# Kernel tuning notes

Hardware: AMD Instinct MI355X
Metric: run time of the kernel (lower is better)

## Reference

```python
import jax, jax.numpy as jnp
import numpy as np

N = 100000      # nodes
E = 1600000     # edges
IN_DIM = 256
H = 128         # hidden_mlp == hidden_gnn
Z = 32          # latent_dim
HD = 128        # hidden_dec


def _lin(k, fan_in, fan_out):
    # torch nn.Linear default init: U(-1/sqrt(fan_in), 1/sqrt(fan_in))
    kw, kb = jax.random.split(k)
    lim = 1.0 / np.sqrt(fan_in)
    W = jax.random.uniform(kw, (fan_in, fan_out), jnp.float32, -lim, lim)
    b = jax.random.uniform(kb, (fan_out,), jnp.float32, -lim, lim)
    return W, b


def setup_inputs() -> dict:
    key = jax.random.key(0)
    ks = jax.random.split(key, 16)
    x = jax.random.normal(ks[0], (N, IN_DIM), jnp.float32)
    edge_index = jax.random.randint(ks[1], (2, E), 0, N, jnp.int64)
    edge_attr = jax.random.uniform(ks[2], (E,), jnp.float32)

    W1, b1 = _lin(ks[3], IN_DIM, H)       # encoder mlp layer 1
    W2, b2 = _lin(ks[4], H, H)            # encoder mlp layer 2
    Wrel1, brel1 = _lin(ks[5], H, H)      # gnn1 lin_rel
    Wroot1, _ = _lin(ks[6], H, H)         # gnn1 lin_root (no bias)
    Wrel2, brel2 = _lin(ks[7], H, H)      # gnn2 lin_rel
    Wroot2, _ = _lin(ks[8], H, H)         # gnn2 lin_root
    Wmu, bmu = _lin(ks[9], H, Z)
    Wlv, blv = _lin(ks[10], H, Z)
    Wd1, bd1 = _lin(ks[11], Z, HD)
    Wd2, bd2 = _lin(ks[12], HD, IN_DIM)
    eps = jax.random.normal(ks[13], (N, Z), jnp.float32)  # reparam noise (fixed)

    return dict(x=x, edge_index=edge_index, edge_attr=edge_attr,
                W1=W1, b1=b1, W2=W2, b2=b2,
                Wrel1=Wrel1, brel1=brel1, Wroot1=Wroot1,
                Wrel2=Wrel2, brel2=brel2, Wroot2=Wroot2,
                Wmu=Wmu, bmu=bmu, Wlv=Wlv, blv=blv,
                Wd1=Wd1, bd1=bd1, Wd2=Wd2, bd2=bd2, eps=eps)


def _graph_conv(h, src, dst, w, Wrel, brel, Wroot):
    # PyG GraphConv (aggr='add'): out_i = lin_rel(sum_{j->i} w_ji * h_j) + lin_root(h_i)
    msgs = h[src] * w[:, None]                       # [E, H] gather
    agg = jax.ops.segment_sum(msgs, dst, num_segments=N)  # [N, H] scatter-add
    return agg @ Wrel + brel + h @ Wroot


def reference(x, edge_index, edge_attr,
              W1, b1, W2, b2,
              Wrel1, brel1, Wroot1,
              Wrel2, brel2, Wroot2,
              Wmu, bmu, Wlv, blv,
              Wd1, bd1, Wd2, bd2, eps):
    src, dst = edge_index[0], edge_index[1]
    # encoder MLP
    h = jax.nn.relu(x @ W1 + b1)
    h = jax.nn.relu(h @ W2 + b2)
    # two GraphConv message-passing layers with ReLU
    h = jax.nn.relu(_graph_conv(h, src, dst, edge_attr, Wrel1, brel1, Wroot1))
    h = jax.nn.relu(_graph_conv(h, src, dst, edge_attr, Wrel2, brel2, Wroot2))
    # heads
    mu = h @ Wmu + bmu
    logvar = h @ Wlv + blv
    # reparameterize with fixed eps
    z = mu + eps * jnp.exp(0.5 * logvar)
    # decoder MLP
    x_recon = jax.nn.relu(z @ Wd1 + bd1) @ Wd2 + bd2
    return x_recon, mu, logvar, z
```

## Files before the change

### kernel.cpp

```cpp
#include <hip/hip_runtime.h>
#include <math.h>

#define NN 100000
#define EE 1600000
#define NB 1563

typedef _Float16 f16;
typedef __attribute__((ext_vector_type(2))) _Float16 f16x2;
typedef __attribute__((ext_vector_type(8))) _Float16 f16x8;
typedef __attribute__((ext_vector_type(4))) float f32x4;
typedef unsigned int u32;

__device__ __forceinline__ float frelu(float v){ return v > 0.f ? v : 0.f; }

__device__ __forceinline__ f32x4 mfma16(f16x8 a, f16x8 b, f32x4 c){
    return __builtin_amdgcn_mfma_f32_16x16x32_f16(a, b, c, 0, 0, 0);
}

__device__ __forceinline__ int2 nt_load_int2(const int2* p){
    long long v = __builtin_nontemporal_load((const long long*)p);
    int2 r; r.x = (int)(v & 0xFFFFFFFFll); r.y = (int)(v >> 32);
    return r;
}

__global__ __launch_bounds__(256) void hist_pack(const int* __restrict__ dst,
                                                 int* __restrict__ blockhist,
                                                 const float* __restrict__ W1,
                                                 const float* __restrict__ W2,
                                                 const float* __restrict__ Wrel1,
                                                 const float* __restrict__ Wroot1,
                                                 const float* __restrict__ Wrel2,
                                                 const float* __restrict__ Wroot2,
                                                 const float* __restrict__ Wd1,
                                                 const float* __restrict__ Wd2,
                                                 const float* __restrict__ Wmu,
                                                 const float* __restrict__ Wlv,
                                                 f16* __restrict__ pack)
{
    __shared__ int cntS[NB];
    const int t = threadIdx.x;
    if (blockIdx.x < 250) {
        const int blk = blockIdx.x;
        for (int i = t; i < NB; i += 256) cntS[i] = 0;
        __syncthreads();
        const int ebase = blk * 6400;
        #pragma unroll
        for (int i = 0; i < 25; i++) {
            int k = dst[ebase + i * 256 + t] >> 6;
            atomicAdd(&cntS[k], 1);
        }
        __syncthreads();
        for (int i = t; i < NB; i += 256)
            blockhist[blk * NB + i] = cntS[i];
        return;
    }
    int tt = (blockIdx.x - 250) * 256 + t;
    float v;
    if (tt < 32768) {
        int l = tt;
        int j = l & 7, lane = (l >> 3) & 63, ct = (l >> 9) & 7, kk = l >> 12;
        int k = kk * 32 + ((lane >> 4) << 3) + j, c = (ct << 4) + (lane & 15);
        v = W1[k * 128 + c];
    } else if (tt < 49152) {
        int l = tt - 32768;
        int j = l & 7, lane = (l >> 3) & 63, ct = (l >> 9) & 7, kk = l >> 12;
        int k = kk * 32 + ((lane >> 4) << 3) + j, c = (ct << 4) + (lane & 15);
        v = W2[k * 128 + c];
    } else if (tt < 81920) {
        int l = tt - 49152;
        int j = l & 7, lane = (l >> 3) & 63, ct = (l >> 9) & 7, kk = l >> 12;
        int k = kk * 32 + ((lane >> 4) << 3) + j, c = (ct << 4) + (lane & 15);
        v = (k < 128) ? Wrel1[k * 128 + c] : Wroot1[(k - 128) * 128 + c];
    } else if (tt < 114688) {
        int l = tt - 81920;
        int j = l & 7, lane = (l >> 3) & 63, ct = (l >> 9) & 7, kk = l >> 12;
        int k = kk * 32 + ((lane >> 4) << 3) + j, c = (ct << 4) + (lane & 15);
        v = (k < 128) ? Wrel2[k * 128 + c] : Wroot2[(k - 128) * 128 + c];
    } else if (tt < 118784) {
        int l = tt - 114688;
        int j = l & 7, lane = (l >> 3) & 63, ct = (l >> 9) & 7;
        int k = ((lane >> 4) << 3) + j, c = (ct << 4) + (lane & 15);
        v = Wd1[k * 128 + c];
    } else if (tt < 151552) {
        int l = tt - 118784;
        int j = l & 7, lane = (l >> 3) & 63, ct = (l >> 9) & 15, kk = l >> 13;
        int k = kk * 32 + ((lane >> 4) << 3) + j, c = (ct << 4) + (lane & 15);
        v = Wd2[k * 256 + c];
    } else {
        int l = tt - 151552;
        int j = l & 7, lane = (l >> 3) & 63, ct = (l >> 9) & 3, kk = l >> 11;
        int k = kk * 32 + ((lane >> 4) << 3) + j, c = (ct << 4) + (lane & 15);
        v = (c < 32) ? Wmu[k * 32 + c] : Wlv[k * 32 + (c - 32)];
    }
    pack[tt] = (f16)v;
}

template<int C>
__device__ __forceinline__ void stage_tile(const float* __restrict__ src, int nbase,
                                           f16* lds, int ldr, int colofs)
{
    const int t = threadIdx.x;
    #pragma unroll
    for (int i = 0; i < (64 * C / 4) / 256; i++) {
        int elem = t + i * 256;
        int row = elem / (C / 4);
        int c4  = elem % (C / 4);
        int srow = nbase + row; if (srow >= NN) srow = NN - 1;
        float4 v = *(const float4*)(src + (size_t)srow * C + c4 * 4);
        union { f16 h[4]; uint2 u; } cv;
        cv.h[0] = (f16)v.x; cv.h[1] = (f16)v.y; cv.h[2] = (f16)v.z; cv.h[3] = (f16)v.w;
        *(uint2*)&lds[row * ldr + colofs + c4 * 4] = cv.u;
    }
}

template<int C>
__device__ __forceinline__ void stage_tile_f16(const f16* __restrict__ src, int nbase,
                                               f16* lds, int ldr, int colofs)
{
    const int t = threadIdx.x;
    #pragma unroll
    for (int i = 0; i < (64 * C / 4) / 256; i++) {
        int elem = t + i * 256;
        int row = elem / (C / 4);
        int c4  = elem % (C / 4);
        int srow = nbase + row; if (srow >= NN) srow = NN - 1;
        uint2 v = *(const uint2*)(src + (size_t)srow * C + c4 * 4);
        *(uint2*)&lds[row * ldr + colofs + c4 * 4] = v;
    }
}

template<int K, int CT>
__device__ __forceinline__ void wave_gemm(const f16* lds, int ldr,
                                          const f16x8* __restrict__ wp, f32x4 acc[CT])
{
    const int lane = threadIdx.x & 63;
    const int wrow = (threadIdx.x >> 6) * 16;
    const int arow = wrow + (lane & 15);
    const int kofs = (lane >> 4) << 3;
    #pragma unroll
    for (int kk = 0; kk < K / 32; kk++) {
        f16x8 a = *(const f16x8*)&lds[arow * ldr + kk * 32 + kofs];
        #pragma unroll
        for (int ct = 0; ct < CT; ct++) {
            f16x8 b = wp[(kk * CT + ct) * 64 + lane];
            acc[ct] = mfma16(a, b, acc[ct]);
        }
    }
}

template<int CT>
__device__ __forceinline__ void zacc(f32x4 acc[CT])
{
    #pragma unroll
    for (int ct = 0; ct < CT; ct++) acc[ct] = f32x4{0.f, 0.f, 0.f, 0.f};
}

template<int CT, bool RELU>
__device__ __forceinline__ void store_f32(float* __restrict__ dst, int OUTC, int nbase,
                                          const float* __restrict__ bias, f32x4 acc[CT])
{
    const int lane = threadIdx.x & 63;
    const int wrow = (threadIdx.x >> 6) * 16;
    #pragma unroll
    for (int ct = 0; ct < CT; ct++) {
        int c = ct * 16 + (lane & 15);
        float bv = bias[c];
        #pragma unroll
        for (int r = 0; r < 4; r++) {
            int node = nbase + wrow + ((lane >> 4) << 2) + r;
            if (node < NN) {
                float v = acc[ct][r] + bv;
                if (RELU) v = frelu(v);
                dst[(size_t)node * OUTC + c] = v;
            }
        }
    }
}

template<int CT, bool RELU>
__device__ __forceinline__ void store_f16g(f16* __restrict__ dst, int OUTC, int nbase,
                                           const float* __restrict__ bias, f32x4 acc[CT])
{
    const int lane = threadIdx.x & 63;
    const int wrow = (threadIdx.x >> 6) * 16;
    #pragma unroll
    for (int ct = 0; ct < CT; ct++) {
        int c = ct * 16 + (lane & 15);
        float bv = bias[c];
        #pragma unroll
        for (int r = 0; r < 4; r++) {
            int node = nbase + wrow + ((lane >> 4) << 2) + r;
            if (node < NN) {
                float v = acc[ct][r] + bv;
                if (RELU) v = frelu(v);
                dst[(size_t)node * OUTC + c] = (f16)v;
            }
        }
    }
}

template<int CT>
__device__ __forceinline__ void store_lds_f16(f16* lds, int ldr,
                                              const float* __restrict__ bias, f32x4 acc[CT])
{
    const int lane = threadIdx.x & 63;
    const int wrow = (threadIdx.x >> 6) * 16;
    #pragma unroll
    for (int ct = 0; ct < CT; ct++) {
        int c = ct * 16 + (lane & 15);
        float bv = bias[c];
        #pragma unroll
        for (int r = 0; r < 4; r++) {
            int row = wrow + ((lane >> 4) << 2) + r;
            lds[row * ldr + c] = (f16)frelu(acc[ct][r] + bv);
        }
    }
}

__global__ __launch_bounds__(256) void colscan_enc(int* __restrict__ blockhist,
                                                   int* __restrict__ totals,
                                                   const float* __restrict__ x,
                                                   const f16x8* __restrict__ wp1,
                                                   const f16x8* __restrict__ wp2,
                                                   const float* __restrict__ b1,
                                                   const float* __restrict__ b2,
                                                   f16* __restrict__ out)
{
    __shared__ __align__(16) f16 shbuf[64 * 264 + 64 * 136];
    const int t = threadIdx.x;
    if (blockIdx.x < NB) {
        int* lds = (int*)shbuf;
        const int k = blockIdx.x;
        int v = (t < 250) ? blockhist[t * NB + k] : 0;
        lds[t] = v;
        __syncthreads();
        for (int off = 1; off < 256; off <<= 1) {
            int y = (t >= off) ? lds[t - off] : 0;
            __syncthreads();
            lds[t] += y;
            __syncthreads();
        }
        if (t < 250) blockhist[t * NB + k] = lds[t] - v;
        if (t == 255) totals[k] = lds[255];
        return;
    }
    f16* xs = shbuf;
    f16* h1 = shbuf + 64 * 264;
    const int nbase = (blockIdx.x - NB) * 64;
    stage_tile<256>(x, nbase, xs, 264, 0);
    __syncthreads();
    f32x4 acc[8];
    zacc<8>(acc);
    wave_gemm<256, 8>(xs, 264, wp1, acc);
    store_lds_f16<8>(h1, 136, b1, acc);
    __syncthreads();
    zacc<8>(acc);
    wave_gemm<128, 8>(h1, 136, wp2, acc);
    store_f16g<8, true>(out, 128, nbase, b2, acc);
}

__global__ __launch_bounds__(256) void scatter(const int* __restrict__ src,
                                               const int* __restrict__ dst,
                                               const float* __restrict__ ea,
                                               const int* __restrict__ totals,
                                               const int* __restrict__ blockhist,
                                               int* __restrict__ bs_g,
                                               int2* __restrict__ tmp)
{
    __shared__ int bsS[NB + 1];
    __shared__ int tmpS[256];
    __shared__ int carryS;
    __shared__ int prefS[NB];
    __shared__ int cntS[NB];
    const int t = threadIdx.x, blk = blockIdx.x;
    if (t == 0) carryS = 0;
    __syncthreads();
    for (int c = 0; c < 7; c++) {
        int idx = c * 256 + t;
        int val = (idx < NB) ? totals[idx] : 0;
        tmpS[t] = val;
        __syncthreads();
        for (int off = 1; off < 256; off <<= 1) {
            int y = (t >= off) ? tmpS[t - off] : 0;
            __syncthreads();
            tmpS[t] += y;
            __syncthreads();
        }
        if (idx < NB) bsS[idx] = carryS + tmpS[t] - val;
        __syncthreads();
        if (t == 255) carryS += tmpS[255];
        __syncthreads();
    }
    if (t == 0) bsS[NB] = carryS;
    for (int i = t; i < NB; i += 256) {
        prefS[i] = blockhist[blk * NB + i];
        cntS[i] = 0;
    }
    __syncthreads();
    if (blk == 0)
        for (int i = t; i < NB + 1; i += 256) bs_g[i] = bsS[i];
    const int ebase = blk * 6400;
    #pragma unroll
    for (int i = 0; i < 25; i++) {
        int e = ebase + i * 256 + t;
        int d = dst[e];
        int k = d >> 6;
        int rank = atomicAdd(&cntS[k], 1);
        int pos = bsS[k] + prefS[k] + rank;
        tmp[pos] = make_int2(src[e] | ((d & 63) << 17), __float_as_int(ea[e]));
    }
}

__global__ __launch_bounds__(256) void bucket_sort(const int2* __restrict__ tmp,
                                                   const int* __restrict__ bs_g,
                                                   int2* __restrict__ pairs,
                                                   int* __restrict__ offsets,
                                                   int* __restrict__ counts)
{
    __shared__ int hist[64], excl[64], cursor[64];
    const int t = threadIdx.x, k = blockIdx.x;
    const int start = bs_g[k], end = bs_g[k + 1];
    if (t < 64) hist[t] = 0;
    __syncthreads();
    for (int i = start + t; i < end; i += 256)
        atomicAdd(&hist[(tmp[i].x >> 17) & 63], 1);
    __syncthreads();
    if (t == 0) {
        int run = 0;
        #pragma unroll
        for (int j = 0; j < 64; j++) { excl[j] = run; cursor[j] = run; run += hist[j]; }
    }
    __syncthreads();
    for (int i = start + t; i < end; i += 256) {
        int2 e = tmp[i];
        int local = (e.x >> 17) & 63;
        int rank = atomicAdd(&cursor[local], 1);
        pairs[start + rank] = make_int2(e.x & 0x1FFFF, e.y);
    }
    if (t < 64) {
        int node = (k << 6) + t;
        if (node < NN) {
            counts[node]  = hist[t];
            offsets[node] = start + excl[t] + hist[t];
        }
    }
}

__global__ __launch_bounds__(256) void agg_q(const f16* __restrict__ h,
                                             const int2* __restrict__ pairs,
                                             const int* __restrict__ offsets,
                                             const int* __restrict__ counts,
                                             f16* __restrict__ out)
{
    const int gt   = blockIdx.x * 256 + threadIdx.x;
    const int node = gt >> 4;
    const int ch   = gt & 15;
    const int end  = offsets[node];
    int i = end - counts[node];
    float acc[8];
    #pragma unroll
    for (int j = 0; j < 8; j++) acc[j] = 0.f;
    const uint4* __restrict__ h16 = (const uint4*)h;
    for (; i + 8 <= end; i += 8) {
        int2 p[8];
        uint4 r[8];
        #pragma unroll
        for (int u = 0; u < 8; u++) p[u] = nt_load_int2(pairs + i + u);
        #pragma unroll
        for (int u = 0; u < 8; u++) r[u] = h16[(size_t)p[u].x * 16 + ch];
        #pragma unroll
        for (int u = 0; u < 8; u++) {
            float w = __int_as_float(p[u].y);
            const f16* e = (const f16*)&r[u];
            #pragma unroll
            for (int j = 0; j < 8; j++) acc[j] = fmaf(w, (float)e[j], acc[j]);
        }
    }
    for (; i + 4 <= end; i += 4) {
        int2 p0 = nt_load_int2(pairs + i);
        int2 p1 = nt_load_int2(pairs + i + 1);
        int2 p2 = nt_load_int2(pairs + i + 2);
        int2 p3 = nt_load_int2(pairs + i + 3);
        uint4 r0 = h16[(size_t)p0.x * 16 + ch];
        uint4 r1 = h16[(size_t)p1.x * 16 + ch];
        uint4 r2 = h16[(size_t)p2.x * 16 + ch];
        uint4 r3 = h16[(size_t)p3.x * 16 + ch];
        float w0 = __int_as_float(p0.y), w1 = __int_as_float(p1.y);
        float w2 = __int_as_float(p2.y), w3 = __int_as_float(p3.y);
        const f16* e0 = (const f16*)&r0;
        const f16* e1 = (const f16*)&r1;
        const f16* e2 = (const f16*)&r2;
        const f16* e3 = (const f16*)&r3;
        #pragma unroll
        for (int j = 0; j < 8; j++) acc[j] = fmaf(w0, (float)e0[j], acc[j]);
        #pragma unroll
        for (int j = 0; j < 8; j++) acc[j] = fmaf(w1, (float)e1[j], acc[j]);
        #pragma unroll
        for (int j = 0; j < 8; j++) acc[j] = fmaf(w2, (float)e2[j], acc[j]);
        #pragma unroll
        for (int j = 0; j < 8; j++) acc[j] = fmaf(w3, (float)e3[j], acc[j]);
    }
    for (; i < end; ++i) {
        int2 p0 = nt_load_int2(pairs + i);
        uint4 r0 = h16[(size_t)p0.x * 16 + ch];
        float w0 = __int_as_float(p0.y);
        const f16* e0 = (const f16*)&r0;
        #pragma unroll
        for (int j = 0; j < 8; j++) acc[j] = fmaf(w0, (float)e0[j], acc[j]);
    }
    union { f16 hh[8]; uint4 u; } cv;
    #pragma unroll
    for (int j = 0; j < 8; j++) cv.hh[j] = (f16)acc[j];
    ((uint4*)out)[(size_t)node * 16 + ch] = cv.u;
}

__global__ __launch_bounds__(256) void conv_mfma(const f16* __restrict__ agg,
                                                 const f16* __restrict__ h,
                                                 const f16x8* __restrict__ wp,
                                                 const float* __restrict__ brel,
                                                 f16* __restrict__ out)
{
    __shared__ __align__(16) f16 as_[64 * 264];
    const int nbase = blockIdx.x * 64;
    stage_tile_f16<128>(agg, nbase, as_, 264, 0);
    stage_tile_f16<128>(h,   nbase, as_, 264, 128);
    __syncthreads();
    f32x4 acc[8];
    zacc<8>(acc);
    wave_gemm<256, 8>(as_, 264, wp, acc);
    store_f16g<8, true>(out, 128, nbase, brel, acc);
}

__global__ __launch_bounds__(256) void tail2_mfma(const f16* __restrict__ h,
                                                  const f16x8* __restrict__ wp_hd,
                                                  const float* __restrict__ bmu,
                                                  const float* __restrict__ blv,
                                                  const f16x8* __restrict__ wp_d1,
                                                  const float* __restrict__ bd1,
                                                  const f16x8* __restrict__ wp_d2,
                                                  const float* __restrict__ bd2,
                                                  const float* __restrict__ eps,
                                                  float* __restrict__ out)
{
    __shared__ __align__(16) f16 hsA[64 * 136];
    __shared__ __align__(16) float muS[64 * 32];
    __shared__ __align__(16) float lvS[64 * 32];
    __shared__ __align__(16) f16 zf[64 * 40];
    const int nbase = blockIdx.x * 64;
    const int t = threadIdx.x;
    const int lane = t & 63;
    const int wrow = (t >> 6) * 16;

    stage_tile_f16<128>(h, nbase, hsA, 136, 0);
    __syncthreads();

    f32x4 acc4[4];
    zacc<4>(acc4);
    wave_gemm<128, 4>(hsA, 136, wp_hd, acc4);
    #pragma unroll
    for (int ct = 0; ct < 4; ct++) {
        int c = ct * 16 + (lane & 15);
        bool ismu = (c < 32);
        int cc = c & 31;
        float bv = ismu ? bmu[cc] : blv[cc];
        float* gbase = out + (ismu ? (size_t)25600000 : (size_t)28800000);
        float* sb = ismu ? muS : lvS;
        #pragma unroll
        for (int r = 0; r < 4; r++) {
            int row = wrow + ((lane >> 4) << 2) + r;
            int node = nbase + row;
            float v = acc4[ct][r] + bv;
            sb[row * 32 + cc] = v;
            if (node < NN) gbase[(size_t)node * 32 + cc] = v;
        }
    }
    __syncthreads();

    {
        const int node = t >> 2;
        const int ch0  = (t & 3) * 8;
        const int gn = nbase + node;
        const float* mu = &muS[node * 32 + ch0];
        const float* lv = &lvS[node * 32 + ch0];
        float4 e0 = make_float4(0.f, 0.f, 0.f, 0.f), e1 = e0;
        if (gn < NN) {
            const size_t g = (size_t)gn * 32 + ch0;
            e0 = *(const float4*)(eps + g);
            e1 = *(const float4*)(eps + g + 4);
        }
        float zv[8];
        zv[0] = fmaf(e0.x, expf(0.5f * lv[0]), mu[0]);
        zv[1] = fmaf(e0.y, expf(0.5f * lv[1]), mu[1]);
        zv[2] = fmaf(e0.z, expf(0.5f * lv[2]), mu[2]);
        zv[3] = fmaf(e0.w, expf(0.5f * lv[3]), mu[3]);
        zv[4] = fmaf(e1.x, expf(0.5f * lv[4]), mu[4]);
        zv[5] = fmaf(e1.y, expf(0.5f * lv[5]), mu[5]);
        zv[6] = fmaf(e1.z, expf(0.5f * lv[6]), mu[6]);
        zv[7] = fmaf(e1.w, expf(0.5f * lv[7]), mu[7]);
        if (gn < NN) {
            const size_t g = (size_t)gn * 32 + ch0;
            *(float4*)(out + 32000000 + g)     = make_float4(zv[0], zv[1], zv[2], zv[3]);
            *(float4*)(out + 32000000 + g + 4) = make_float4(zv[4], zv[5], zv[6], zv[7]);
        }
        #pragma unroll
        for (int j = 0; j < 8; j++) zf[node * 40 + ch0 + j] = (f16)zv[j];
    }
    __syncthreads();

    f32x4 acc8[8];
    zacc<8>(acc8);
    wave_gemm<32, 8>(zf, 40, wp_d1, acc8);
    store_lds_f16<8>(hsA, 136, bd1, acc8);
    __syncthreads();

    f32x4 acc16[16];
    zacc<16>(acc16);
    wave_gemm<128, 16>(hsA, 136, wp_d2, acc16);
    store_f32<16, false>(out, 256, nbase, bd2, acc16);
}

extern "C" void kernel_launch(void* const* d_in, const int* in_sizes, int n_in,
                              void* d_out, int out_size, void* d_ws, size_t ws_size,
                              hipStream_t stream)
{
    const float* x     = (const float*)d_in[0];
    const int*   ei    = (const int*)d_in[1];
    const float* ea    = (const float*)d_in[2];
    const float* W1    = (const float*)d_in[3];
    const float* b1    = (const float*)d_in[4];
    const float* W2    = (const float*)d_in[5];
    const float* b2    = (const float*)d_in[6];
    const float* Wrel1 = (const float*)d_in[7];
    const float* brel1 = (const float*)d_in[8];
    const float* Wroot1= (const float*)d_in[9];
    const float* Wrel2 = (const float*)d_in[10];
    const float* brel2 = (const float*)d_in[11];
    const float* Wroot2= (const float*)d_in[12];
    const float* Wmu   = (const float*)d_in[13];
    const float* bmu   = (const float*)d_in[14];
    const float* Wlv   = (const float*)d_in[15];
    const float* blv   = (const float*)d_in[16];
    const float* Wd1   = (const float*)d_in[17];
    const float* bd1   = (const float*)d_in[18];
    const float* Wd2   = (const float*)d_in[19];
    const float* bd2   = (const float*)d_in[20];
    const float* eps   = (const float*)d_in[21];
    float* out = (float*)d_out;

    char* ws = (char*)d_ws;
    int*  totals    = (int*) (ws);
    int*  blockhist = (int*) (ws + 8192);
    int*  bs_g      = (int*) (ws + 1571200);
    int2* tmp       = (int2*)(ws + 1577472);
    int2* pairs     = (int2*)(ws + 14377472);
    int*  offsets   = (int*) (ws + 27177472);
    int*  counts    = (int*) (ws + 27577472);
    f16*  pack      = (f16*) (ws + 27977472);
    f16*  B0        = (f16*) (ws + 28311552);
    f16*  B1        = (f16*) (ws + 53911552);

    const f16x8* wp_enc1  = (const f16x8*)(pack);
    const f16x8* wp_enc2  = (const f16x8*)(pack + 32768);
    const f16x8* wp_conv1 = (const f16x8*)(pack + 49152);
    const f16x8* wp_conv2 = (const f16x8*)(pack + 81920);
    const f16x8* wp_dec1  = (const f16x8*)(pack + 114688);
    const f16x8* wp_dec2  = (const f16x8*)(pack + 118784);
    const f16x8* wp_heads = (const f16x8*)(pack + 151552);

    const int* src = ei;
    const int* dst = ei + EE;

    hist_pack<<<874, 256, 0, stream>>>(dst, blockhist, W1, W2, Wrel1, Wroot1,
                                       Wrel2, Wroot2, Wd1, Wd2, Wmu, Wlv, pack);
    colscan_enc<<<NB + 1563, 256, 0, stream>>>(blockhist, totals, x,
                                               wp_enc1, wp_enc2, b1, b2, B0);
    scatter<<<250, 256, 0, stream>>>(src, dst, ea, totals, blockhist, bs_g, tmp);
    bucket_sort<<<NB, 256, 0, stream>>>(tmp, bs_g, pairs, offsets, counts);

    agg_q<<<6250, 256, 0, stream>>>(B0, pairs, offsets, counts, B1);
    conv_mfma<<<1563, 256, 0, stream>>>(B1, B0, wp_conv1, brel1, B1);
    agg_q<<<6250, 256, 0, stream>>>(B1, pairs, offsets, counts, B0);
    conv_mfma<<<1563, 256, 0, stream>>>(B0, B1, wp_conv2, brel2, B0);
    tail2_mfma<<<1563, 256, 0, stream>>>(B0, wp_heads, bmu, blv,
                                         wp_dec1, bd1, wp_dec2, bd2, eps, out);
}
```

Before: 385.7 us.

## Batch column scan over 16 buckets per block with segmented LDS scan

The column-wise exclusive scan of the block histogram now handles 16 bucket columns per workgroup instead of one, which cuts the scan-side grid from 1563 blocks to 98. Each block loads a padded 250x16 tile, splits the rows into 16 segments per column, sums each segment, scans the segment totals, then rescans within each segment. This removes the many strided single-column loads and the log-step barrier loop of the old version. The cost is more serial per-thread work and fewer blocks to overlap with the encoder GEMM blocks in the same launch.

```diff
diff --git a/kernel.cpp b/kernel.cpp
--- a/kernel.cpp
+++ b/kernel.cpp
@@ -4,6 +4,7 @@
 #define NN 100000
 #define EE 1600000
 #define NB 1563
+#define NCB 98
 
 typedef _Float16 f16;
 typedef __attribute__((ext_vector_type(2))) _Float16 f16x2;
@@ -228,25 +229,51 @@
 {
     __shared__ __align__(16) f16 shbuf[64 * 264 + 64 * 136];
     const int t = threadIdx.x;
-    if (blockIdx.x < NB) {
-        int* lds = (int*)shbuf;
-        const int k = blockIdx.x;
-        int v = (t < 250) ? blockhist[t * NB + k] : 0;
-        lds[t] = v;
-        __syncthreads();
-        for (int off = 1; off < 256; off <<= 1) {
-            int y = (t >= off) ? lds[t - off] : 0;
-            __syncthreads();
-            lds[t] += y;
-            __syncthreads();
-        }
-        if (t < 250) blockhist[t * NB + k] = lds[t] - v;
-        if (t == 255) totals[k] = lds[255];
+    if (blockIdx.x < NCB) {
+        int* hsI  = (int*)shbuf;
+        int* segS = hsI + 250 * 17;
+        const int k0 = blockIdx.x * 16;
+        for (int idx = t; idx < 250 * 16; idx += 256) {
+            int row = idx >> 4, col = idx & 15;
+            int k = k0 + col;
+            hsI[row * 17 + col] = (k < NB) ? blockhist[row * NB + k] : 0;
+        }
+        __syncthreads();
+        const int col = t & 15, seg = t >> 4;
+        const int r0 = seg * 16;
+        const int r1 = (r0 + 16 < 250) ? r0 + 16 : 250;
+        int s = 0;
+        for (int r = r0; r < r1; r++) s += hsI[r * 17 + col];
+        segS[seg * 17 + col] = s;
+        __syncthreads();
+        if (t < 16) {
+            int run = 0;
+            #pragma unroll
+            for (int g = 0; g < 16; g++) {
+                int tmp = segS[g * 17 + t];
+                segS[g * 17 + t] = run;
+                run += tmp;
+            }
+            if (k0 + t < NB) totals[k0 + t] = run;
+        }
+        __syncthreads();
+        int run = segS[seg * 17 + col];
+        for (int r = r0; r < r1; r++) {
+            int old = hsI[r * 17 + col];
+            hsI[r * 17 + col] = run;
+            run += old;
+        }
+        __syncthreads();
+        for (int idx = t; idx < 250 * 16; idx += 256) {
+            int row = idx >> 4, col2 = idx & 15;
+            int k = k0 + col2;
+            if (k < NB) blockhist[row * NB + k] = hsI[row * 17 + col2];
+        }
         return;
     }
     f16* xs = shbuf;
     f16* h1 = shbuf + 64 * 264;
-    const int nbase = (blockIdx.x - NB) * 64;
+    const int nbase = (blockIdx.x - NCB) * 64;
     stage_tile<256>(x, nbase, xs, 264, 0);
     __syncthreads();
     f32x4 acc[8];
@@ -572,8 +599,8 @@
 
     hist_pack<<<874, 256, 0, stream>>>(dst, blockhist, W1, W2, Wrel1, Wroot1,
                                        Wrel2, Wroot2, Wd1, Wd2, Wmu, Wlv, pack);
-    colscan_enc<<<NB + 1563, 256, 0, stream>>>(blockhist, totals, x,
-                                               wp_enc1, wp_enc2, b1, b2, B0);
+    colscan_enc<<<NCB + 1563, 256, 0, stream>>>(blockhist, totals, x,
+                                                wp_enc1, wp_enc2, b1, b2, B0);
     scatter<<<250, 256, 0, stream>>>(src, dst, ea, totals, blockhist, bs_g, tmp);
     bucket_sort<<<NB, 256, 0, stream>>>(tmp, bs_g, pairs, offsets, counts);
 
```

After: 377.1 us (median of 2 runs). -2.2%, faster.
